# Kernel optimization log

Hardware: AMD Instinct MI355X
Metric: run time of the kernel (lower is better)

The kernel has to match this reference:

```python
import jax, jax.numpy as jnp
import numpy as np
from math import factorial, pi, sqrt

LMAX = 5
MUL_IN = 128
NUM_CHANNELS = 4
NUM_RADII = 20
RES_BETA = 180
RES_ALPHA = 359
IRREPS_DIM = (LMAX + 1) ** 2  # 36
NUM_GRAPHS = 32
NUM_SPECIES = 5


def _sh_grid_matrix():
    """Real spherical harmonics evaluated on a Gauss-Legendre (beta) x uniform (alpha) grid.

    Returns Y of shape [RES_BETA, RES_ALPHA, IRREPS_DIM]; this is the dense form of
    e3nn's to_s2grid (Legendre x Fourier) transform matrix.
    """
    y, _ = np.polynomial.legendre.leggauss(RES_BETA)  # y = cos(beta), quadrature='gausslegendre'
    alpha = 2.0 * np.pi * np.arange(RES_ALPHA) / RES_ALPHA
    # Associated Legendre P_l^m(y) (no Condon-Shortley), shape [l, m, RES_BETA]
    P = np.zeros((LMAX + 1, LMAX + 1, RES_BETA))
    P[0, 0] = 1.0
    sy = np.sqrt(np.maximum(1.0 - y * y, 0.0))
    for m in range(1, LMAX + 1):
        P[m, m] = (2 * m - 1) * sy * P[m - 1, m - 1]
    for m in range(LMAX):
        P[m + 1, m] = (2 * m + 1) * y * P[m, m]
    for m in range(LMAX + 1):
        for l in range(m + 2, LMAX + 1):
            P[l, m] = ((2 * l - 1) * y * P[l - 1, m] - (l + m - 1) * P[l - 2, m]) / (l - m)
    Y = np.zeros((RES_BETA, RES_ALPHA, IRREPS_DIM))
    idx = 0
    for l in range(LMAX + 1):
        for m in range(-l, l + 1):
            am = abs(m)
            K = sqrt((2 * l + 1) / (4.0 * pi) * factorial(l - am) / factorial(l + am))
            if m == 0:
                Y[:, :, idx] = (K * P[l, 0])[:, None]
            elif m > 0:
                Y[:, :, idx] = sqrt(2.0) * K * P[l, m][:, None] * np.cos(m * alpha)[None, :]
            else:
                Y[:, :, idx] = sqrt(2.0) * K * P[l, am][:, None] * np.sin(am * alpha)[None, :]
            idx += 1
    return Y.astype(np.float32)


def setup_inputs() -> dict:
    key = jax.random.key(0)
    k1, k2, k3, k4 = jax.random.split(key, 4)
    focus = jax.random.normal(k1, (NUM_GRAPHS, MUL_IN * IRREPS_DIM), dtype=jnp.float32)
    embed_table = jax.random.normal(k2, (NUM_SPECIES, MUL_IN * (LMAX + 1)), dtype=jnp.float32)
    linear_weights = jax.random.normal(k3, (LMAX + 1, MUL_IN, NUM_RADII * NUM_CHANNELS), dtype=jnp.float32)
    target_species = jax.random.randint(k4, (NUM_GRAPHS,), 0, NUM_SPECIES)
    return {
        "focus_node_embeddings": focus,
        "embed_table": embed_table,
        "linear_weights": linear_weights,
        "target_species": target_species,
    }


def reference(focus_node_embeddings, embed_table, linear_weights, target_species):
    G = focus_node_embeddings.shape[0]
    Y = jnp.asarray(_sh_grid_matrix())  # [B, A, 36]
    emb = embed_table[target_species]  # [G, num_irreps = 768], one scalar per irrep channel
    inv_sqrt_fan = 1.0 / np.sqrt(MUL_IN).astype(np.float32)

    coeffs = []
    off_in, off_emb = 0, 0
    for l in range(LMAX + 1):
        dim_m = 2 * l + 1
        # irreps-block view: [G, mul_in, 2l+1]
        x_l = focus_node_embeddings[:, off_in:off_in + MUL_IN * dim_m].reshape(G, MUL_IN, dim_m)
        # per-irrep scalar gating (target_species_embeddings * focus_node_embeddings)
        x_l = x_l * emb[:, off_emb:off_emb + MUL_IN, None]
        # equivariant Linear: mixes multiplicities only, per m, fan-in normalized
        y_l = jnp.einsum("gim,io->gom", x_l, linear_weights[l]) * inv_sqrt_fan
        # mul_to_axis(num_channels) then mul_to_axis(num_radii)
        coeffs.append(y_l.reshape(G, NUM_CHANNELS, NUM_RADII, dim_m))
        off_in += MUL_IN * dim_m
        off_emb += MUL_IN
    position_coeffs = jnp.concatenate(coeffs, axis=-1)  # [G, C, R, 36]

    # to_s2grid: coefficients -> spherical grid signal
    grid = jnp.einsum("gcri,bai->gcrba", position_coeffs, Y)  # [G, C, R, B, A]
    # logsumexp over channels, then max-normalize per graph
    logits = jax.scipy.special.logsumexp(grid, axis=1)  # [G, R, B, A]
    logits = logits - logits.max(axis=(-3, -2, -1), keepdims=True)
    return position_coeffs, logits
```

## Files before the change

### kernel.cpp

```cpp
#include <hip/hip_runtime.h>

#define G_N    32
#define MUL    128
#define RADII  20
#define CH     4
#define RES_B  180
#define RES_A  359
#define IDIM   36
#define COEFF_N (G_N*CH*RADII*IDIM)
#define PER_G   (RADII*RES_B*RES_A)
#define PER_G4  (PER_G/4)
#define NCHUNK 3
#define BCH_BLK 60
#define BCH_W   15

typedef float v2f __attribute__((ext_vector_type(2)));

__device__ __forceinline__ float fexp2(float x){
#if __has_builtin(__builtin_amdgcn_exp2f)
  return __builtin_amdgcn_exp2f(x);
#else
  return exp2f(x);
#endif
}
__device__ __forceinline__ float flog2(float x){
#if __has_builtin(__builtin_amdgcn_logf)
  return __builtin_amdgcn_logf(x);
#else
  return log2f(x);
#endif
}
__device__ __forceinline__ unsigned enc_f(float f){
  unsigned u = __float_as_uint(f);
  return (u & 0x80000000u) ? ~u : (u | 0x80000000u);
}
__device__ __forceinline__ float dec_f(unsigned k){
  return __uint_as_float((k & 0x80000000u) ? (k ^ 0x80000000u) : ~k);
}

__global__ __launch_bounds__(256) void fused_prep_kernel(
                              const float* __restrict__ focus, const float* __restrict__ embt,
                              const float* __restrict__ W, const int* __restrict__ tspec,
                              float* __restrict__ out,
                              float* __restrict__ PYs, float* __restrict__ Ftab){
  __shared__ double ak[RES_B + 1], bk[RES_B + 1];
  int blk = blockIdx.x;
  int t   = threadIdx.x;
  if (blk == 360){
    const double PI = 3.14159265358979323846;
    const double LOG2E = 1.4426950408889634074;
    if (t >= 2 && t <= RES_B){
      ak[t] = (2.0*t - 1.0) / (double)t;
      bk[t] = (t - 1.0) / (double)t;
    }
    __syncthreads();
    if (t < RES_B){
      int i = RES_B - 1 - t;
      double x = cos(PI * (i + 0.75) / (RES_B + 0.5));
      for (int it = 0; it < 5; ++it){
        double p0 = 1.0, p1 = x;
        for (int k = 2; k <= RES_B; ++k){
          double t1 = ak[k] * x;
          double pk = fma(t1, p1, -(bk[k] * p0));
          p0 = p1; p1 = pk;
        }
        x -= p1 * (x*x - 1.0) / ((double)RES_B * (x*p1 - p0));
      }
      double y = x;
      double sy = sqrt(fmax(1.0 - y*y, 0.0));
      double P[6][6];
      P[0][0] = 1.0;
      for (int m = 1; m < 6; ++m) P[m][m] = (2.0*m - 1.0)*sy*P[m-1][m-1];
      for (int m = 0; m < 5; ++m) P[m+1][m] = (2.0*m + 1.0)*y*P[m][m];
      for (int m = 0; m < 6; ++m)
        for (int l = m + 2; l < 6; ++l)
          P[l][m] = ((2.0*l - 1.0)*y*P[l-1][m] - (l + m - 1.0)*P[l-2][m]) / (double)(l - m);
      const double fact[11] = {1,1,2,6,24,120,720,5040,40320,362880,3628800};
      for (int l = 0; l < 6; ++l)
        for (int m = 0; m <= l; ++m){
          double K = sqrt((2.0*l + 1.0)/(4.0*PI)*fact[l-m]/fact[l+m]);
          double v = K * P[l][m] * LOG2E;
          if (m > 0) v *= sqrt(2.0);
          PYs[t*36 + l*6 + m] = (float)v;
        }
    }
    for (int a = t; a < RES_A; a += 256){
      double al = 2.0*PI*a/(double)RES_A;
      Ftab[a*12 + 0] = 1.0f;
      for (int m = 1; m <= 5; ++m){
        Ftab[a*12 + m]     = (float)cos(m*al);
        Ftab[a*12 + 5 + m] = (float)sin(m*al);
      }
      Ftab[a*12 + 11] = 0.f;
    }
  } else {
    int idx = blk * 256 + t;
    int i36 = idx % IDIM;
    int go  = idx / IDIM;
    int o   = go % (CH*RADII);
    int g   = go / (CH*RADII);
    int l   = (int)sqrtf((float)i36 + 0.5f);
    int mo  = i36 - l*l;
    int dim = 2*l + 1;
    const float* fp = focus + g*(MUL*IDIM) + MUL*l*l + mo;
    const float* ep = embt + tspec[g]*(MUL*6) + MUL*l;
    const float* wp = W + l*(MUL*80) + o;
    float s = 0.f;
    #pragma unroll 4
    for (int i = 0; i < MUL; ++i)
      s = fmaf(fp[i*dim] * ep[i], wp[i*80], s);
    out[idx] = s * 0.088388347648318447f;
  }
}

__global__ __launch_bounds__(256, 4) void compute_kernel(const float* __restrict__ coeffs,
                          const float* __restrict__ PYs, const float* __restrict__ Ftab,
                          float* __restrict__ out, unsigned* __restrict__ gmax){
  int blk   = blockIdx.x;
  int chunk = blk % NCHUNK;
  int gr    = blk / NCHUNK;
  int r = gr % RADII;
  int g = gr / RADII;
  int tid  = threadIdx.x;
  int wave = tid >> 6, lane = tid & 63;
  int b0   = chunk * BCH_BLK;

  __shared__ float cv[CH][IDIM];
  __shared__ __align__(16) float tmpa[BCH_BLK][12][4];
  __shared__ float wred[4];

  for (int v = tid; v < CH*IDIM; v += 256){
    int c = v / IDIM, i = v % IDIM;
    cv[c][i] = coeffs[((g*CH + c)*RADII + r)*IDIM + i];
  }
  float f0[11], f1[11], f2[11];
  {
    const float4* Fq = reinterpret_cast<const float4*>(Ftab);
    float4 a0 = Fq[lane*3],       a1 = Fq[lane*3+1],       a2 = Fq[lane*3+2];
    float4 b0v = Fq[(lane+64)*3], b1 = Fq[(lane+64)*3+1],  b2 = Fq[(lane+64)*3+2];
    float4 c0 = Fq[(lane+128)*3], c1 = Fq[(lane+128)*3+1], c2 = Fq[(lane+128)*3+2];
    f0[0]=a0.x; f0[1]=a0.y; f0[2]=a0.z; f0[3]=a0.w; f0[4]=a1.x; f0[5]=a1.y;
    f0[6]=a1.z; f0[7]=a1.w; f0[8]=a2.x; f0[9]=a2.y; f0[10]=a2.z;
    f1[0]=b0v.x; f1[1]=b0v.y; f1[2]=b0v.z; f1[3]=b0v.w; f1[4]=b1.x; f1[5]=b1.y;
    f1[6]=b1.z; f1[7]=b1.w; f1[8]=b2.x; f1[9]=b2.y; f1[10]=b2.z;
    f2[0]=c0.x; f2[1]=c0.y; f2[2]=c0.z; f2[3]=c0.w; f2[4]=c1.x; f2[5]=c1.y;
    f2[6]=c1.z; f2[7]=c1.w; f2[8]=c2.x; f2[9]=c2.y; f2[10]=c2.z;
  }
  __syncthreads();

  for (int v = tid; v < BCH_BLK*44; v += 256){
    int bl = v / 44, cm = v % 44;
    int c = cm / 11, mm = cm % 11;
    int am, ii;
    if (mm == 0)      { am = 0;      ii = 0;        }
    else if (mm <= 5) { am = mm;     ii = mm;       }
    else              { am = mm - 5; ii = -(mm-5);  }
    const float* py = PYs + (b0 + bl)*36 + am;
    float s = 0.f;
    for (int l = am; l < 6; ++l)
      s = fmaf(cv[c][l*l + l + ii], py[l*6], s);
    tmpa[bl][mm][c] = s;
  }
  __syncthreads();

  float smax = 0.f;
  float* row = out + ((size_t)gr*RES_B + b0 + wave*BCH_W)*RES_A;
  for (int bl = 0; bl < BCH_W; ++bl){
    const float4* tq = reinterpret_cast<const float4*>(&tmpa[wave*BCH_W + bl][0][0]);
    float4 q[11];
    #pragma unroll
    for (int mm = 0; mm < 11; ++mm) q[mm] = tq[mm];
    #pragma unroll
    for (int k = 0; k < 3; ++k){
      if (k == 2 && lane >= 52) break;
      const float* fr = (k == 0) ? f0 : (k == 1) ? f1 : f2;
      int p = lane + 64*k;
      v2f C01 = {q[0].x, q[0].y}, C23 = {q[0].z, q[0].w};
      #pragma unroll
      for (int mm = 1; mm <= 5; ++mm){
        v2f fs = {fr[mm], fr[mm]};
        C01 = __builtin_elementwise_fma((v2f){q[mm].x, q[mm].y}, fs, C01);
        C23 = __builtin_elementwise_fma((v2f){q[mm].z, q[mm].w}, fs, C23);
      }
      v2f f6 = {fr[6], fr[6]};
      v2f S01 = (v2f){q[6].x, q[6].y} * f6, S23 = (v2f){q[6].z, q[6].w} * f6;
      #pragma unroll
      for (int mm = 7; mm <= 10; ++mm){
        v2f fs = {fr[mm], fr[mm]};
        S01 = __builtin_elementwise_fma((v2f){q[mm].x, q[mm].y}, fs, S01);
        S23 = __builtin_elementwise_fma((v2f){q[mm].z, q[mm].w}, fs, S23);
      }
      v2f hp01 = C01 + S01, hp23 = C23 + S23;
      v2f hm01 = C01 - S01, hm23 = C23 - S23;
      float sp = (fexp2(hp01.x) + fexp2(hp01.y)) + (fexp2(hp23.x) + fexp2(hp23.y));
      float sm = (fexp2(hm01.x) + fexp2(hm01.y)) + (fexp2(hm23.x) + fexp2(hm23.y));
      row[p] = sp;
      if (p) row[359 - p] = sm;
      smax = fmaxf(smax, fmaxf(sp, sm));
    }
    row += RES_A;
  }
  #pragma unroll
  for (int off = 32; off > 0; off >>= 1)
    smax = fmaxf(smax, __shfl_xor(smax, off, 64));
  if (lane == 0) wred[wave] = smax;
  __syncthreads();
  if (tid == 0){
    float m = fmaxf(fmaxf(wred[0], wred[1]), fmaxf(wred[2], wred[3]));
    atomicMax(gmax + g, enc_f(m));
  }
}

__global__ __launch_bounds__(256) void fixup_kernel(float* __restrict__ logits,
                                                    const unsigned* __restrict__ gmax){
  const float LN2 = 0.69314718055994531f;
  const int total4 = G_N * PER_G4;
  float4* l4 = reinterpret_cast<float4*>(logits);
  int stride = gridDim.x * 256;
  for (int i = blockIdx.x * 256 + threadIdx.x; i < total4; i += stride){
    int g = (int)(((unsigned)i) / PER_G4);
    float nsub = -flog2(dec_f(gmax[g])) * LN2;
    float4 v = l4[i];
    v.x = fmaf(flog2(v.x), LN2, nsub);
    v.y = fmaf(flog2(v.y), LN2, nsub);
    v.z = fmaf(flog2(v.z), LN2, nsub);
    v.w = fmaf(flog2(v.w), LN2, nsub);
    l4[i] = v;
  }
}

extern "C" void kernel_launch(void* const* d_in, const int* in_sizes, int n_in,
                              void* d_out, int out_size, void* d_ws, size_t ws_size,
                              hipStream_t stream){
  const float* focus = (const float*)d_in[0];
  const float* embt  = (const float*)d_in[1];
  const float* W     = (const float*)d_in[2];
  const int*   tspec = (const int*)d_in[3];
  float* out = (float*)d_out;
  float* ws  = (float*)d_ws;
  unsigned* gmax = (unsigned*)d_ws;
  float* PYs  = ws + 32;
  float* Ftab = ws + 32 + RES_B*36;

  hipMemsetAsync(d_ws, 0, 128, stream);
  fused_prep_kernel<<<361, 256, 0, stream>>>(focus, embt, W, tspec, out, PYs, Ftab);
  float* logits = out + COEFF_N;
  compute_kernel<<<G_N*RADII*NCHUNK, 256, 0, stream>>>(out, PYs, Ftab, logits, gmax);
  fixup_kernel<<<2048, 256, 0, stream>>>(logits, gmax);
}
```

Baseline: 156.8 us.

## Recompute grid in two passes instead of write-then-fixup of logits

Replaces the store-then-fixup scheme with two launches of a templated compute kernel. The first pass only computes the per-graph max, with no global writes. The second pass recomputes the grid values and writes the final normalized log values directly. This removes the full read-modify-write pass over the large logits array at the cost of doing the grid arithmetic and exp twice. It also rebalances the chunking (5 chunks of 36 beta rows) and reassociates the FMA chains for more instruction-level parallelism.

```diff
diff --git a/kernel.cpp b/kernel.cpp
--- a/kernel.cpp
+++ b/kernel.cpp
@@ -8,11 +8,9 @@
 #define RES_A  359
 #define IDIM   36
 #define COEFF_N (G_N*CH*RADII*IDIM)
-#define PER_G   (RADII*RES_B*RES_A)
-#define PER_G4  (PER_G/4)
-#define NCHUNK 3
-#define BCH_BLK 60
-#define BCH_W   15
+#define NCHUNK 5
+#define BCH_BLK 36
+#define BCH_W   9
 
 typedef float v2f __attribute__((ext_vector_type(2)));
 
@@ -113,6 +111,7 @@
   }
 }
 
+template<int WRITE>
 __global__ __launch_bounds__(256, 4) void compute_kernel(const float* __restrict__ coeffs,
                           const float* __restrict__ PYs, const float* __restrict__ Ftab,
                           float* __restrict__ out, unsigned* __restrict__ gmax){
@@ -133,6 +132,8 @@
     int c = v / IDIM, i = v % IDIM;
     cv[c][i] = coeffs[((g*CH + c)*RADII + r)*IDIM + i];
   }
+  float nsub = 0.f;
+  if (WRITE) nsub = -flog2(dec_f(gmax[g])) * 0.69314718055994531f;
   float f0[11], f1[11], f2[11];
   {
     const float4* Fq = reinterpret_cast<const float4*>(Ftab);
@@ -163,6 +164,7 @@
   }
   __syncthreads();
 
+  const float LN2 = 0.69314718055994531f;
   float smax = 0.f;
   float* row = out + ((size_t)gr*RES_B + b0 + wave*BCH_W)*RES_A;
   for (int bl = 0; bl < BCH_W; ++bl){
@@ -175,57 +177,49 @@
       if (k == 2 && lane >= 52) break;
       const float* fr = (k == 0) ? f0 : (k == 1) ? f1 : f2;
       int p = lane + 64*k;
-      v2f C01 = {q[0].x, q[0].y}, C23 = {q[0].z, q[0].w};
-      #pragma unroll
-      for (int mm = 1; mm <= 5; ++mm){
-        v2f fs = {fr[mm], fr[mm]};
-        C01 = __builtin_elementwise_fma((v2f){q[mm].x, q[mm].y}, fs, C01);
-        C23 = __builtin_elementwise_fma((v2f){q[mm].z, q[mm].w}, fs, C23);
-      }
-      v2f f6 = {fr[6], fr[6]};
-      v2f S01 = (v2f){q[6].x, q[6].y} * f6, S23 = (v2f){q[6].z, q[6].w} * f6;
-      #pragma unroll
-      for (int mm = 7; mm <= 10; ++mm){
-        v2f fs = {fr[mm], fr[mm]};
-        S01 = __builtin_elementwise_fma((v2f){q[mm].x, q[mm].y}, fs, S01);
-        S23 = __builtin_elementwise_fma((v2f){q[mm].z, q[mm].w}, fs, S23);
-      }
+      #define PK(i) (v2f){q[i].x, q[i].y}
+      #define PK2(i) (v2f){q[i].z, q[i].w}
+      #define FS(i) (v2f){fr[i], fr[i]}
+      v2f ca0 = __builtin_elementwise_fma(PK(1), FS(1), PK(0));
+      v2f ca1 = __builtin_elementwise_fma(PK2(1), FS(1), PK2(0));
+      v2f cb0 = __builtin_elementwise_fma(PK(3), FS(3), PK(2) * FS(2));
+      v2f cb1 = __builtin_elementwise_fma(PK2(3), FS(3), PK2(2) * FS(2));
+      v2f cc0 = __builtin_elementwise_fma(PK(5), FS(5), PK(4) * FS(4));
+      v2f cc1 = __builtin_elementwise_fma(PK2(5), FS(5), PK2(4) * FS(4));
+      v2f C01 = (ca0 + cb0) + cc0;
+      v2f C23 = (ca1 + cb1) + cc1;
+      v2f sa0 = __builtin_elementwise_fma(PK(7), FS(7), PK(6) * FS(6));
+      v2f sa1 = __builtin_elementwise_fma(PK2(7), FS(7), PK2(6) * FS(6));
+      v2f sb0 = __builtin_elementwise_fma(PK(9), FS(9), PK(8) * FS(8));
+      v2f sb1 = __builtin_elementwise_fma(PK2(9), FS(9), PK2(8) * FS(8));
+      v2f S01 = (sa0 + sb0) + PK(10) * FS(10);
+      v2f S23 = (sa1 + sb1) + PK2(10) * FS(10);
+      #undef PK
+      #undef PK2
+      #undef FS
       v2f hp01 = C01 + S01, hp23 = C23 + S23;
       v2f hm01 = C01 - S01, hm23 = C23 - S23;
       float sp = (fexp2(hp01.x) + fexp2(hp01.y)) + (fexp2(hp23.x) + fexp2(hp23.y));
       float sm = (fexp2(hm01.x) + fexp2(hm01.y)) + (fexp2(hm23.x) + fexp2(hm23.y));
-      row[p] = sp;
-      if (p) row[359 - p] = sm;
-      smax = fmaxf(smax, fmaxf(sp, sm));
+      if (WRITE){
+        row[p] = fmaf(flog2(sp), LN2, nsub);
+        if (p) row[359 - p] = fmaf(flog2(sm), LN2, nsub);
+      } else {
+        smax = fmaxf(smax, fmaxf(sp, sm));
+      }
     }
     row += RES_A;
   }
-  #pragma unroll
-  for (int off = 32; off > 0; off >>= 1)
-    smax = fmaxf(smax, __shfl_xor(smax, off, 64));
-  if (lane == 0) wred[wave] = smax;
-  __syncthreads();
-  if (tid == 0){
-    float m = fmaxf(fmaxf(wred[0], wred[1]), fmaxf(wred[2], wred[3]));
-    atomicMax(gmax + g, enc_f(m));
-  }
-}
-
-__global__ __launch_bounds__(256) void fixup_kernel(float* __restrict__ logits,
-                                                    const unsigned* __restrict__ gmax){
-  const float LN2 = 0.69314718055994531f;
-  const int total4 = G_N * PER_G4;
-  float4* l4 = reinterpret_cast<float4*>(logits);
-  int stride = gridDim.x * 256;
-  for (int i = blockIdx.x * 256 + threadIdx.x; i < total4; i += stride){
-    int g = (int)(((unsigned)i) / PER_G4);
-    float nsub = -flog2(dec_f(gmax[g])) * LN2;
-    float4 v = l4[i];
-    v.x = fmaf(flog2(v.x), LN2, nsub);
-    v.y = fmaf(flog2(v.y), LN2, nsub);
-    v.z = fmaf(flog2(v.z), LN2, nsub);
-    v.w = fmaf(flog2(v.w), LN2, nsub);
-    l4[i] = v;
+  if (!WRITE){
+    #pragma unroll
+    for (int off = 32; off > 0; off >>= 1)
+      smax = fmaxf(smax, __shfl_xor(smax, off, 64));
+    if (lane == 0) wred[wave] = smax;
+    __syncthreads();
+    if (tid == 0){
+      float m = fmaxf(fmaxf(wred[0], wred[1]), fmaxf(wred[2], wred[3]));
+      atomicMax(gmax + g, enc_f(m));
+    }
   }
 }
 
@@ -245,6 +239,6 @@
   hipMemsetAsync(d_ws, 0, 128, stream);
   fused_prep_kernel<<<361, 256, 0, stream>>>(focus, embt, W, tspec, out, PYs, Ftab);
   float* logits = out + COEFF_N;
-  compute_kernel<<<G_N*RADII*NCHUNK, 256, 0, stream>>>(out, PYs, Ftab, logits, gmax);
-  fixup_kernel<<<2048, 256, 0, stream>>>(logits, gmax);
-}
+  compute_kernel<0><<<G_N*RADII*NCHUNK, 256, 0, stream>>>(out, PYs, Ftab, logits, gmax);
+  compute_kernel<1><<<G_N*RADII*NCHUNK, 256, 0, stream>>>(out, PYs, Ftab, logits, gmax);
+}
```

After: 165.9 us. +5.8%, slower.
